# Kernel tuning notes

Hardware: AMD Instinct MI355X
Metric: run time of the kernel (lower is better)

Reference implementation:

```python
import jax, jax.numpy as jnp
import numpy as np

N_HEADS = 16
HIDDEN = 1024
HEAD_DIM = 64
BSZ = 4
SEQ = 1024
SCALE = HEAD_DIM ** -0.5


def setup_inputs() -> dict:
    key = jax.random.key(0)
    k_x, k_q, k_k, k_v, k_o = jax.random.split(key, 5)
    s = HIDDEN ** -0.5
    return {
        "x": jax.random.normal(k_x, (BSZ, SEQ, HIDDEN), dtype=jnp.float32),
        # torch nn.Linear weights: shape (out_features, in_features)
        "wq": jax.random.normal(k_q, (N_HEADS * HEAD_DIM, HIDDEN), dtype=jnp.float32) * s,
        "wk": jax.random.normal(k_k, (N_HEADS * HEAD_DIM, HIDDEN), dtype=jnp.float32) * s,
        "wv": jax.random.normal(k_v, (N_HEADS * HEAD_DIM, HIDDEN), dtype=jnp.float32) * s,
        "wo": jax.random.normal(k_o, (HIDDEN, N_HEADS * HEAD_DIM), dtype=jnp.float32) * s,
    }


def reference(x, wq, wk, wv, wo):
    bsz, seqlen, _ = x.shape
    xq = jnp.einsum("bsh,oh->bso", x, wq)  # (b, s, n_heads*head_dim)
    xk = jnp.einsum("bsh,oh->bso", x, wk)
    xv = jnp.einsum("bsh,oh->bso", x, wv)
    # Faithful to the original: raw view to (b, n_heads, s, head_dim), NO transpose
    xq = xq.reshape(bsz, N_HEADS, seqlen, HEAD_DIM)
    xk = xk.reshape(bsz, N_HEADS, seqlen, HEAD_DIM)
    xv = xv.reshape(bsz, N_HEADS, seqlen, HEAD_DIM)
    scores = jnp.einsum("bhid,bhjd->bhij", xq, xk) * SCALE
    scores = jax.nn.softmax(scores, axis=-1)
    out = jnp.einsum("bhij,bhjd->bhid", scores, xv)
    out = out.reshape(bsz, seqlen, N_HEADS * HEAD_DIM)  # raw view, faithful
    return jnp.einsum("bso,ho->bsh", out, wo)
```

## Files before the change

kernel.cpp:

```cpp
#include <hip/hip_runtime.h>
#include <hip/hip_bf16.h>

typedef __hip_bfloat16 bf16;
typedef __attribute__((ext_vector_type(8))) short short8;
typedef __attribute__((ext_vector_type(4))) short short4v;
typedef __attribute__((ext_vector_type(4))) float f32x4;


__device__ __forceinline__ short f2b(float x) {
    bf16 h = __float2bfloat16(x);
    return *reinterpret_cast<short*>(&h);
}
__device__ __forceinline__ f32x4 zero4() {
    f32x4 z; z[0] = 0.f; z[1] = 0.f; z[2] = 0.f; z[3] = 0.f; return z;
}
__device__ __forceinline__ void gl_lds16(const void* g, void* l) {
    __builtin_amdgcn_global_load_lds(
        (const __attribute__((address_space(1))) void*)g,
        (__attribute__((address_space(3))) void*)l, 16, 0, 0);
}

__global__ __launch_bounds__(256) void convert_in(const float* __restrict__ w0,
                                                  const float* __restrict__ w1,
                                                  const float* __restrict__ w2,
                                                  const float* __restrict__ w3,
                                                  const float* __restrict__ x,
                                                  bf16* __restrict__ Wb,
                                                  bf16* __restrict__ Xb) {
    const int y = blockIdx.y;
    const float* s;
    bf16* d;
    if (y < 4) {
        s = (y == 0) ? w0 : (y == 1) ? w1 : (y == 2) ? w2 : w3;
        d = Wb + (size_t)y * 1048576;
    } else {
        s = x + (size_t)(y - 4) * 1048576;
        d = Xb + (size_t)(y - 4) * 1048576;
    }
    const int i = (blockIdx.x * 256 + threadIdx.x) * 4;
    const float4 v = *(const float4*)(s + i);
    short4v o;
    o[0] = f2b(v.x); o[1] = f2b(v.y); o[2] = f2b(v.z); o[3] = f2b(v.w);
    *(short4v*)(d + i) = o;
}

__global__ __launch_bounds__(256) void gemm_qkv(const bf16* __restrict__ Xb,
                                                const bf16* __restrict__ Wb,
                                                bf16* __restrict__ QK,
                                                bf16* __restrict__ VT) {
    __shared__ __align__(16) bf16 As[128 * 32];
    __shared__ __align__(16) bf16 Bs[128 * 32];

    const int tid  = threadIdx.x;
    const int wave = tid >> 6;
    const int lane = tid & 63;
    const int z    = blockIdx.z;
    const int bm   = blockIdx.x * 128, bn = blockIdx.y * 128;
    const bf16* Bsrc = Wb + (size_t)z * 1048576;

    const int f0 = wave * 2048 + lane * 16, f1 = f0 + 1024;
    const char* gA0 = (const char*)(Xb + (size_t)(bm + (f0 >> 6)) * 1024) + (f0 & 63);
    const char* gA1 = (const char*)(Xb + (size_t)(bm + (f1 >> 6)) * 1024) + (f1 & 63);
    const char* gB0 = (const char*)(Bsrc + (size_t)(bn + (f0 >> 6)) * 1024) + (f0 & 63);
    const char* gB1 = (const char*)(Bsrc + (size_t)(bn + (f1 >> 6)) * 1024) + (f1 & 63);
    char* lA0 = (char*)As + wave * 2048;      char* lA1 = lA0 + 1024;
    char* lB0 = (char*)Bs + wave * 2048;      char* lB1 = lB0 + 1024;

    f32x4 acc[4][4];
#pragma unroll
    for (int i = 0; i < 4; i++)
#pragma unroll
        for (int j = 0; j < 4; j++) acc[i][j] = zero4();

    const int mrow = ((wave >> 1) * 64) + (lane & 15);
    const int nrow = ((wave & 1) * 64) + (lane & 15);
    const int kcol = (lane >> 4) * 8;

    for (int k0 = 0; k0 < 1024; k0 += 32) {
        __syncthreads();
        gl_lds16(gA0 + (size_t)k0 * 2, lA0);
        gl_lds16(gA1 + (size_t)k0 * 2, lA1);
        gl_lds16(gB0 + (size_t)k0 * 2, lB0);
        gl_lds16(gB1 + (size_t)k0 * 2, lB1);
        __syncthreads();
        short8 af[4], bfr[4];
#pragma unroll
        for (int i = 0; i < 4; i++)
            af[i] = *(const short8*)&As[(mrow + i * 16) * 32 + kcol];
#pragma unroll
        for (int j = 0; j < 4; j++)
            bfr[j] = *(const short8*)&Bs[(nrow + j * 16) * 32 + kcol];
#pragma unroll
        for (int i = 0; i < 4; i++)
#pragma unroll
            for (int j = 0; j < 4; j++)
                acc[i][j] = __builtin_amdgcn_mfma_f32_16x16x32_bf16(
                    af[i], bfr[j], acc[i][j], 0, 0, 0);
    }

    const int erow = bm + (wave >> 1) * 64 + (lane >> 4) * 4;
    const int ecol = bn + (wave & 1) * 64 + (lane & 15);
    if (z < 2) {
        bf16* C = QK + (size_t)z * 4194304;
#pragma unroll
        for (int i = 0; i < 4; i++)
#pragma unroll
            for (int j = 0; j < 4; j++)
#pragma unroll
                for (int r = 0; r < 4; r++)
                    C[(size_t)(erow + i * 16 + r) * 1024 + (ecol + j * 16)] =
                        __float2bfloat16(acc[i][j][r]);
    } else {
#pragma unroll
        for (int i = 0; i < 4; i++)
#pragma unroll
            for (int j = 0; j < 4; j++) {
                const int o  = ecol + j * 16;
                const int d  = o & 63;
                const int oh = o >> 6;
#pragma unroll
                for (int r = 0; r < 4; r++) {
                    const int rr = erow + i * 16 + r;
                    VT[(size_t)(rr >> 6) * 65536 + d * 1024 +
                       ((rr & 63) * 16 + oh)] = __float2bfloat16(acc[i][j][r]);
                }
            }
    }
}

__global__ __launch_bounds__(256) void gemm_out(const bf16* __restrict__ A,
                                                const bf16* __restrict__ B,
                                                float* __restrict__ C) {
    __shared__ __align__(16) bf16 As[128 * 32];
    __shared__ __align__(16) bf16 Bs[64 * 32];

    const int tid  = threadIdx.x;
    const int wave = tid >> 6;
    const int lane = tid & 63;
    const int bm   = blockIdx.x * 128, bn = blockIdx.y * 64;

    const int f0 = wave * 2048 + lane * 16, f1 = f0 + 1024;
    const int fB = tid * 16;
    const char* gA0 = (const char*)(A + (size_t)(bm + (f0 >> 6)) * 1024) + (f0 & 63);
    const char* gA1 = (const char*)(A + (size_t)(bm + (f1 >> 6)) * 1024) + (f1 & 63);
    const char* gB0 = (const char*)(B + (size_t)(bn + (fB >> 6)) * 1024) + (fB & 63);
    char* lA0 = (char*)As + f0;
    char* lA1 = (char*)As + f1;
    char* lB0 = (char*)Bs + fB;

    f32x4 acc[4][2];
#pragma unroll
    for (int i = 0; i < 4; i++)
#pragma unroll
        for (int j = 0; j < 2; j++) acc[i][j] = zero4();

    const int mrow = ((wave >> 1) * 64) + (lane & 15);
    const int nrow = ((wave & 1) * 32) + (lane & 15);
    const int kcol = (lane >> 4) * 8;

    for (int k0 = 0; k0 < 1024; k0 += 32) {
        __syncthreads();
        gl_lds16(gA0 + (size_t)k0 * 2, lA0);
        gl_lds16(gA1 + (size_t)k0 * 2, lA1);
        gl_lds16(gB0 + (size_t)k0 * 2, lB0);
        __syncthreads();
        short8 af[4], bfr[2];
#pragma unroll
        for (int i = 0; i < 4; i++)
            af[i] = *(const short8*)&As[(mrow + i * 16) * 32 + kcol];
#pragma unroll
        for (int j = 0; j < 2; j++)
            bfr[j] = *(const short8*)&Bs[(nrow + j * 16) * 32 + kcol];
#pragma unroll
        for (int i = 0; i < 4; i++)
#pragma unroll
            for (int j = 0; j < 2; j++)
                acc[i][j] = __builtin_amdgcn_mfma_f32_16x16x32_bf16(
                    af[i], bfr[j], acc[i][j], 0, 0, 0);
    }

    const int erow = bm + (wave >> 1) * 64 + (lane >> 4) * 4;
    const int ecol = bn + (wave & 1) * 32 + (lane & 15);
#pragma unroll
    for (int i = 0; i < 4; i++)
#pragma unroll
        for (int j = 0; j < 2; j++)
#pragma unroll
            for (int r = 0; r < 4; r++)
                C[(size_t)(erow + i * 16 + r) * 1024 + (ecol + j * 16)] =
                    acc[i][j][r];
}

#define PSTR 72
__global__ __launch_bounds__(256) void attn(bf16* __restrict__ QO,
                                            const bf16* __restrict__ K,
                                            const bf16* __restrict__ VT) {
    __shared__ __align__(16) bf16 Ks[64 * 64];
    __shared__ __align__(16) bf16 Vs[64 * 64];
    __shared__ __align__(16) bf16 Ps[128 * PSTR];

    const int tid  = threadIdx.x;
    const int wave = tid >> 6;
    const int lane = tid & 63;
    const int lg   = lane >> 4;
    const int li   = lane & 15;

    const int head = blockIdx.x >> 3;
    const int qt   = blockIdx.x & 7;
    bf16* Qh = QO + (size_t)head * 65536 + qt * 8192;
    const char* Khb  = (const char*)(K + (size_t)head * 65536);
    const char* VThb = (const char*)(VT + (size_t)head * 65536);

    short8 qf[2][2];
#pragma unroll
    for (int i = 0; i < 2; i++)
#pragma unroll
        for (int ks = 0; ks < 2; ks++)
            qf[i][ks] = *(const short8*)&Qh[(wave * 32 + i * 16 + li) * 64 +
                                            ks * 32 + lg * 8];

    f32x4 o_acc[2][4];
    float lp[2][4];
#pragma unroll
    for (int i = 0; i < 2; i++) {
#pragma unroll
        for (int j = 0; j < 4; j++) o_acc[i][j] = zero4();
#pragma unroll
        for (int r = 0; r < 4; r++) lp[i][r] = 0.f;
    }

    const int fs0 = wave * 2048 + lane * 16, fs1 = fs0 + 1024;
    char* lK0 = (char*)Ks + fs0;   char* lK1 = (char*)Ks + fs1;
    char* lV0 = (char*)Vs + fs0;   char* lV1 = (char*)Vs + fs1;
    const char* gV0 = VThb + (size_t)(fs0 >> 7) * 2048 + (fs0 & 127);
    const char* gV1 = VThb + (size_t)(fs1 >> 7) * 2048 + (fs1 & 127);

    for (int jt = 0; jt < 16; jt++) {
        __syncthreads();
        gl_lds16(Khb + (size_t)jt * 8192 + fs0, lK0);
        gl_lds16(Khb + (size_t)jt * 8192 + fs1, lK1);
        gl_lds16(gV0 + jt * 128, lV0);
        gl_lds16(gV1 + jt * 128, lV1);
        __syncthreads();

        f32x4 s_acc[2][4];
#pragma unroll
        for (int i = 0; i < 2; i++)
#pragma unroll
            for (int j = 0; j < 4; j++) s_acc[i][j] = zero4();
#pragma unroll
        for (int j = 0; j < 4; j++)
#pragma unroll
            for (int ks = 0; ks < 2; ks++) {
                short8 kf = *(const short8*)&Ks[(j * 16 + li) * 64 + ks * 32 + lg * 8];
#pragma unroll
                for (int i = 0; i < 2; i++)
                    s_acc[i][j] = __builtin_amdgcn_mfma_f32_16x16x32_bf16(
                        qf[i][ks], kf, s_acc[i][j], 0, 0, 0);
            }

#pragma unroll
        for (int i = 0; i < 2; i++)
#pragma unroll
            for (int r = 0; r < 4; r++) {
                const int prow = wave * 32 + i * 16 + lg * 4 + r;
                float ps = 0.f;
#pragma unroll
                for (int j = 0; j < 4; j++) {
                    const float p = __expf(s_acc[i][j][r] * 0.125f);
                    ps += p;
                    Ps[prow * PSTR + j * 16 + li] = __float2bfloat16(p);
                }
                lp[i][r] += ps;
            }

#pragma unroll
        for (int ks = 0; ks < 2; ks++) {
            short8 pa[2];
#pragma unroll
            for (int i = 0; i < 2; i++)
                pa[i] = *(const short8*)&Ps[(wave * 32 + i * 16 + li) * PSTR +
                                            ks * 32 + lg * 8];
#pragma unroll
            for (int jd = 0; jd < 4; jd++) {
                short8 vf = *(const short8*)&Vs[(jd * 16 + li) * 64 + ks * 32 + lg * 8];
#pragma unroll
                for (int i = 0; i < 2; i++)
                    o_acc[i][jd] = __builtin_amdgcn_mfma_f32_16x16x32_bf16(
                        pa[i], vf, o_acc[i][jd], 0, 0, 0);
            }
        }
    }

#pragma unroll
    for (int i = 0; i < 2; i++)
#pragma unroll
        for (int r = 0; r < 4; r++) {
            float l = lp[i][r];
#pragma unroll
            for (int off = 1; off < 16; off <<= 1) l += __shfl_xor(l, off, 16);
            const float inv = 1.f / l;
#pragma unroll
            for (int jd = 0; jd < 4; jd++)
                Qh[(wave * 32 + i * 16 + lg * 4 + r) * 64 + jd * 16 + li] =
                    __float2bfloat16(o_acc[i][jd][r] * inv);
        }
}

extern "C" void kernel_launch(void* const* d_in, const int* in_sizes, int n_in,
                              void* d_out, int out_size, void* d_ws, size_t ws_size,
                              hipStream_t stream) {
    const float* x  = (const float*)d_in[0];
    const float* wq = (const float*)d_in[1];
    const float* wk = (const float*)d_in[2];
    const float* wv = (const float*)d_in[3];
    const float* wo = (const float*)d_in[4];

    bf16* ws = (bf16*)d_ws;
    bf16* Wb = ws;
    bf16* QK = ws + 4194304;
    bf16* VT = ws + 12582912;
    bf16* Xb = (bf16*)d_out;

    convert_in<<<dim3(1024, 8), 256, 0, stream>>>(wq, wk, wv, wo, x, Wb, Xb);
    gemm_qkv<<<dim3(32, 8, 3), 256, 0, stream>>>(Xb, Wb, QK, VT);
    attn<<<512, 256, 0, stream>>>(QK, QK + 4194304, VT);
    gemm_out<<<dim3(32, 16), 256, 0, stream>>>(QK, Wb + 3145728, (float*)d_out);
}
```

Baseline: 188.7 us.

## Rewrite QKV GEMM as 256x256 8-wave kernel with double-buffered swizzled LDS

Replaces the 128x128 QKV projection GEMM with a 256x256-tile, 512-thread kernel that double-buffers 64-wide K slices in 128KB of LDS. It uses an XOR swizzle to avoid bank conflicts and splits each K step into four phases that interleave global-to-LDS prefetch with MFMA work, using manual barriers, waitcnts and setprio. The goal is to overlap memory latency with compute and raise data reuse per block compared with the fully synchronous single-buffer loop. The trade-off is a much smaller grid (192 blocks), heavy register and LDS use that may limit occupancy, and fragile hand-written synchronisation.

```diff
diff --git a/kernel.cpp b/kernel.cpp
--- a/kernel.cpp
+++ b/kernel.cpp
@@ -44,87 +44,128 @@
     *(short4v*)(d + i) = o;
 }
 
-__global__ __launch_bounds__(256) void gemm_qkv(const bf16* __restrict__ Xb,
-                                                const bf16* __restrict__ Wb,
-                                                bf16* __restrict__ QK,
-                                                bf16* __restrict__ VT) {
-    __shared__ __align__(16) bf16 As[128 * 32];
-    __shared__ __align__(16) bf16 Bs[128 * 32];
+#define PH(MQ, NQ, READA, SG, SLOFF, VM) do {                                  \
+    if (READA) {                                                               \
+      _Pragma("unroll") for (int i = 0; i < 4; ++i)                            \
+      _Pragma("unroll") for (int ks = 0; ks < 2; ++ks)                         \
+        af[i][ks] = *(const short8*)(ldsb + d + (MQ)*16384 +                   \
+            (((wr*64 + i*16 + li)*64 + ((ks*32 + lg*8) ^ swz)) << 1));         \
+    }                                                                          \
+    _Pragma("unroll") for (int j = 0; j < 2; ++j)                              \
+    _Pragma("unroll") for (int ks = 0; ks < 2; ++ks)                           \
+      bfr[j][ks] = *(const short8*)(ldsb + d + 32768 + (NQ)*16384 +            \
+          (((wc*32 + j*16 + li)*64 + ((ks*32 + lg*8) ^ swz)) << 1));           \
+    gl_lds16(SG + (size_t)ktn * 64, ldsw + dn + (SLOFF));                      \
+    gl_lds16(SG + (size_t)ktn * 64 + 65536, ldsw + dn + (SLOFF) + 8192);       \
+    asm volatile("" ::: "memory");                                             \
+    __builtin_amdgcn_s_barrier();                                              \
+    asm volatile("s_waitcnt lgkmcnt(0)" ::: "memory");                         \
+    __builtin_amdgcn_sched_barrier(0);                                         \
+    __builtin_amdgcn_s_setprio(1);                                             \
+    _Pragma("unroll") for (int i = 0; i < 4; ++i)                              \
+    _Pragma("unroll") for (int j = 0; j < 2; ++j)                              \
+    _Pragma("unroll") for (int ks = 0; ks < 2; ++ks)                           \
+      acc[(MQ)*4 + i][(NQ)*2 + j] = __builtin_amdgcn_mfma_f32_16x16x32_bf16(   \
+          af[i][ks], bfr[j][ks], acc[(MQ)*4 + i][(NQ)*2 + j], 0, 0, 0);        \
+    __builtin_amdgcn_s_setprio(0);                                             \
+    if (VM) asm volatile("s_waitcnt vmcnt(4)" ::: "memory");                   \
+    __builtin_amdgcn_s_barrier();                                              \
+  } while (0)
+
+__global__ __launch_bounds__(512, 2) void gemm_qkv8(const bf16* __restrict__ Xb,
+                                                    const bf16* __restrict__ Wb,
+                                                    bf16* __restrict__ QK,
+                                                    bf16* __restrict__ VT) {
+    __shared__ __align__(16) bf16 lds[65536];
 
     const int tid  = threadIdx.x;
-    const int wave = tid >> 6;
+    const int w    = tid >> 6;
     const int lane = tid & 63;
+    const int wr   = w >> 2;
+    const int wc   = w & 3;
+    const int li   = lane & 15;
+    const int lg   = lane >> 4;
+    const int swz  = (li & 7) << 3;
     const int z    = blockIdx.z;
-    const int bm   = blockIdx.x * 128, bn = blockIdx.y * 128;
+    const int bm   = blockIdx.x * 256, bn = blockIdx.y * 256;
     const bf16* Bsrc = Wb + (size_t)z * 1048576;
 
-    const int f0 = wave * 2048 + lane * 16, f1 = f0 + 1024;
-    const char* gA0 = (const char*)(Xb + (size_t)(bm + (f0 >> 6)) * 1024) + (f0 & 63);
-    const char* gA1 = (const char*)(Xb + (size_t)(bm + (f1 >> 6)) * 1024) + (f1 & 63);
-    const char* gB0 = (const char*)(Bsrc + (size_t)(bn + (f0 >> 6)) * 1024) + (f0 & 63);
-    const char* gB1 = (const char*)(Bsrc + (size_t)(bn + (f1 >> 6)) * 1024) + (f1 & 63);
-    char* lA0 = (char*)As + wave * 2048;      char* lA1 = lA0 + 1024;
-    char* lB0 = (char*)Bs + wave * 2048;      char* lB1 = lB0 + 1024;
-
-    f32x4 acc[4][4];
-#pragma unroll
-    for (int i = 0; i < 4; i++)
-#pragma unroll
-        for (int j = 0; j < 4; j++) acc[i][j] = zero4();
-
-    const int mrow = ((wave >> 1) * 64) + (lane & 15);
-    const int nrow = ((wave & 1) * 64) + (lane & 15);
-    const int kcol = (lane >> 4) * 8;
-
-    for (int k0 = 0; k0 < 1024; k0 += 32) {
-        __syncthreads();
-        gl_lds16(gA0 + (size_t)k0 * 2, lA0);
-        gl_lds16(gA1 + (size_t)k0 * 2, lA1);
-        gl_lds16(gB0 + (size_t)k0 * 2, lB0);
-        gl_lds16(gB1 + (size_t)k0 * 2, lB1);
-        __syncthreads();
-        short8 af[4], bfr[4];
-#pragma unroll
-        for (int i = 0; i < 4; i++)
-            af[i] = *(const short8*)&As[(mrow + i * 16) * 32 + kcol];
-#pragma unroll
-        for (int j = 0; j < 4; j++)
-            bfr[j] = *(const short8*)&Bs[(nrow + j * 16) * 32 + kcol];
-#pragma unroll
-        for (int i = 0; i < 4; i++)
-#pragma unroll
-            for (int j = 0; j < 4; j++)
-                acc[i][j] = __builtin_amdgcn_mfma_f32_16x16x32_bf16(
-                    af[i], bfr[j], acc[i][j], 0, 0, 0);
-    }
-
-    const int erow = bm + (wave >> 1) * 64 + (lane >> 4) * 4;
-    const int ecol = bn + (wave & 1) * 64 + (lane & 15);
+    const int srow = w * 8 + (lane >> 3);
+    const int scol = ((lane & 7) ^ (lane >> 3)) * 8;
+    const bf16* gA0 = Xb   + (size_t)(bm + srow) * 1024 + scol;
+    const bf16* gB0 = Bsrc + (size_t)(bn + srow) * 1024 + scol;
+    const bf16* gA1 = gA0 + 131072;
+    const bf16* gB1 = gB0 + 131072;
+    const char* ldsb = (const char*)lds;
+    char* ldsw = (char*)lds + w * 1024;
+
+    f32x4 acc[8][4];
+#pragma unroll
+    for (int i = 0; i < 8; ++i)
+#pragma unroll
+        for (int j = 0; j < 4; ++j) acc[i][j] = zero4();
+
+    short8 af[4][2], bfr[2][2];
+
+    {
+        gl_lds16(gA0, ldsw + 0);      gl_lds16(gA0 + 65536, ldsw + 8192);
+        gl_lds16(gB0, ldsw + 32768);  gl_lds16(gB0 + 65536, ldsw + 40960);
+        gl_lds16(gB1, ldsw + 49152);  gl_lds16(gB1 + 65536, ldsw + 57344);
+        gl_lds16(gA1, ldsw + 16384);  gl_lds16(gA1 + 65536, ldsw + 24576);
+        asm volatile("s_waitcnt vmcnt(4)" ::: "memory");
+        __builtin_amdgcn_s_barrier();
+    }
+
+    for (int kt = 0; kt < 16; ++kt) {
+        const int d   = (kt & 1) << 16;
+        const int dn  = ((kt + 1) & 1) << 16;
+        const int ktn = (kt < 15) ? kt + 1 : 0;
+        PH(0, 0, 1, gA0, 0,     1);
+        PH(0, 1, 0, gB0, 32768, 1);
+        PH(1, 0, 1, gB1, 49152, 0);
+        PH(1, 1, 0, gA1, 16384, 1);
+    }
+
+    asm volatile("s_waitcnt vmcnt(0)" ::: "memory");
+
     if (z < 2) {
         bf16* C = QK + (size_t)z * 4194304;
 #pragma unroll
-        for (int i = 0; i < 4; i++)
-#pragma unroll
-            for (int j = 0; j < 4; j++)
-#pragma unroll
-                for (int r = 0; r < 4; r++)
-                    C[(size_t)(erow + i * 16 + r) * 1024 + (ecol + j * 16)] =
-                        __float2bfloat16(acc[i][j][r]);
+        for (int mq = 0; mq < 2; ++mq)
+#pragma unroll
+        for (int i = 0; i < 4; ++i)
+#pragma unroll
+        for (int nq = 0; nq < 2; ++nq)
+#pragma unroll
+        for (int j = 0; j < 2; ++j) {
+            const int gr0 = bm + mq * 128 + wr * 64 + i * 16 + lg * 4;
+            const int gc  = bn + nq * 128 + wc * 32 + j * 16 + li;
+#pragma unroll
+            for (int r = 0; r < 4; ++r)
+                C[(size_t)(gr0 + r) * 1024 + gc] =
+                    __float2bfloat16(acc[mq * 4 + i][nq * 2 + j][r]);
+        }
     } else {
 #pragma unroll
-        for (int i = 0; i < 4; i++)
-#pragma unroll
-            for (int j = 0; j < 4; j++) {
-                const int o  = ecol + j * 16;
-                const int d  = o & 63;
-                const int oh = o >> 6;
-#pragma unroll
-                for (int r = 0; r < 4; r++) {
-                    const int rr = erow + i * 16 + r;
-                    VT[(size_t)(rr >> 6) * 65536 + d * 1024 +
-                       ((rr & 63) * 16 + oh)] = __float2bfloat16(acc[i][j][r]);
-                }
+        for (int mq = 0; mq < 2; ++mq)
+#pragma unroll
+        for (int i = 0; i < 4; ++i)
+#pragma unroll
+        for (int nq = 0; nq < 2; ++nq)
+#pragma unroll
+        for (int j = 0; j < 2; ++j) {
+            const int gr0 = bm + mq * 128 + wr * 64 + i * 16 + lg * 4;
+            const int o   = bn + nq * 128 + wc * 32 + j * 16 + li;
+            const int dd  = o & 63;
+            const int oh  = o >> 6;
+#pragma unroll
+            for (int r = 0; r < 4; ++r) {
+                const int rr = gr0 + r;
+                VT[(size_t)(rr >> 6) * 65536 + dd * 1024 +
+                   ((rr & 63) * 16 + oh)] =
+                    __float2bfloat16(acc[mq * 4 + i][nq * 2 + j][r]);
             }
+        }
     }
 }
 
@@ -323,7 +364,7 @@
     bf16* Xb = (bf16*)d_out;
 
     convert_in<<<dim3(1024, 8), 256, 0, stream>>>(wq, wk, wv, wo, x, Wb, Xb);
-    gemm_qkv<<<dim3(32, 8, 3), 256, 0, stream>>>(Xb, Wb, QK, VT);
+    gemm_qkv8<<<dim3(16, 4, 3), 512, 0, stream>>>(Xb, Wb, QK, VT);
     attn<<<512, 256, 0, stream>>>(QK, QK + 4194304, VT);
     gemm_out<<<dim3(32, 16), 256, 0, stream>>>(QK, Wb + 3145728, (float*)d_out);
 }
```

After: 204.7 us. 1.08x slower.

## Triple-buffer LDS tiles in QKV and output GEMMs with async prefetch

Applied to the files above, without the earlier changes.

Both GEMM kernels now keep three LDS stages and issue global-to-LDS loads two k-tiles ahead. A partial vmcnt wait plus a single barrier per iteration replaces the two __syncthreads, so loads can overlap the MFMA work. The cost is triple the LDS footprint per block, which may lower occupancy. The loads wrap around to k-tile 0/1 at the end, doing redundant work that is only drained afterwards.

```diff
diff --git a/kernel.cpp b/kernel.cpp
--- a/kernel.cpp
+++ b/kernel.cpp
@@ -48,8 +48,8 @@
                                                 const bf16* __restrict__ Wb,
                                                 bf16* __restrict__ QK,
                                                 bf16* __restrict__ VT) {
-    __shared__ __align__(16) bf16 As[128 * 32];
-    __shared__ __align__(16) bf16 Bs[128 * 32];
+    __shared__ __align__(16) bf16 As[3][128 * 32];
+    __shared__ __align__(16) bf16 Bs[3][128 * 32];
 
     const int tid  = threadIdx.x;
     const int wave = tid >> 6;
@@ -63,8 +63,15 @@
     const char* gA1 = (const char*)(Xb + (size_t)(bm + (f1 >> 6)) * 1024) + (f1 & 63);
     const char* gB0 = (const char*)(Bsrc + (size_t)(bn + (f0 >> 6)) * 1024) + (f0 & 63);
     const char* gB1 = (const char*)(Bsrc + (size_t)(bn + (f1 >> 6)) * 1024) + (f1 & 63);
-    char* lA0 = (char*)As + wave * 2048;      char* lA1 = lA0 + 1024;
-    char* lB0 = (char*)Bs + wave * 2048;      char* lB1 = lB0 + 1024;
+    char* Ab = (char*)As;
+    char* Bb = (char*)Bs;
+
+#define QKV_STAGE(BUF, KB) do {                                   \
+        gl_lds16(gA0 + (KB), Ab + (BUF) + f0);                    \
+        gl_lds16(gA1 + (KB), Ab + (BUF) + f1);                    \
+        gl_lds16(gB0 + (KB), Bb + (BUF) + f0);                    \
+        gl_lds16(gB1 + (KB), Bb + (BUF) + f1);                    \
+    } while (0)
 
     f32x4 acc[4][4];
 #pragma unroll
@@ -76,27 +83,35 @@
     const int nrow = ((wave & 1) * 64) + (lane & 15);
     const int kcol = (lane >> 4) * 8;
 
-    for (int k0 = 0; k0 < 1024; k0 += 32) {
-        __syncthreads();
-        gl_lds16(gA0 + (size_t)k0 * 2, lA0);
-        gl_lds16(gA1 + (size_t)k0 * 2, lA1);
-        gl_lds16(gB0 + (size_t)k0 * 2, lB0);
-        gl_lds16(gB1 + (size_t)k0 * 2, lB1);
-        __syncthreads();
+    QKV_STAGE(0, 0);
+    QKV_STAGE(8192, 64);
+
+    int bR = 0, bS = 16384;
+    for (int kt = 0; kt < 32; ++kt) {
+        asm volatile("s_waitcnt vmcnt(4)" ::: "memory");
+        __builtin_amdgcn_s_barrier();
+        const int kb = ((kt + 2) & 31) * 64;
+        QKV_STAGE(bS, kb);
         short8 af[4], bfr[4];
 #pragma unroll
         for (int i = 0; i < 4; i++)
-            af[i] = *(const short8*)&As[(mrow + i * 16) * 32 + kcol];
+            af[i] = *(const short8*)(Ab + bR +
+                        (((mrow + i * 16) * 32 + kcol) << 1));
 #pragma unroll
         for (int j = 0; j < 4; j++)
-            bfr[j] = *(const short8*)&Bs[(nrow + j * 16) * 32 + kcol];
+            bfr[j] = *(const short8*)(Bb + bR +
+                        (((nrow + j * 16) * 32 + kcol) << 1));
 #pragma unroll
         for (int i = 0; i < 4; i++)
 #pragma unroll
             for (int j = 0; j < 4; j++)
                 acc[i][j] = __builtin_amdgcn_mfma_f32_16x16x32_bf16(
                     af[i], bfr[j], acc[i][j], 0, 0, 0);
-    }
+        bR = (bR == 16384) ? 0 : bR + 8192;
+        bS = (bS == 16384) ? 0 : bS + 8192;
+    }
+    asm volatile("s_waitcnt vmcnt(0)" ::: "memory");
+#undef QKV_STAGE
 
     const int erow = bm + (wave >> 1) * 64 + (lane >> 4) * 4;
     const int ecol = bn + (wave & 1) * 64 + (lane & 15);
@@ -131,8 +146,8 @@
 __global__ __launch_bounds__(256) void gemm_out(const bf16* __restrict__ A,
                                                 const bf16* __restrict__ B,
                                                 float* __restrict__ C) {
-    __shared__ __align__(16) bf16 As[128 * 32];
-    __shared__ __align__(16) bf16 Bs[64 * 32];
+    __shared__ __align__(16) bf16 As[3][128 * 32];
+    __shared__ __align__(16) bf16 Bs[3][64 * 32];
 
     const int tid  = threadIdx.x;
     const int wave = tid >> 6;
@@ -144,9 +159,14 @@
     const char* gA0 = (const char*)(A + (size_t)(bm + (f0 >> 6)) * 1024) + (f0 & 63);
     const char* gA1 = (const char*)(A + (size_t)(bm + (f1 >> 6)) * 1024) + (f1 & 63);
     const char* gB0 = (const char*)(B + (size_t)(bn + (fB >> 6)) * 1024) + (fB & 63);
-    char* lA0 = (char*)As + f0;
-    char* lA1 = (char*)As + f1;
-    char* lB0 = (char*)Bs + fB;
+    char* Ab = (char*)As;
+    char* Bb = (char*)Bs;
+
+#define OUT_STAGE(BA, BB, KB) do {                                \
+        gl_lds16(gA0 + (KB), Ab + (BA) + f0);                     \
+        gl_lds16(gA1 + (KB), Ab + (BA) + f1);                     \
+        gl_lds16(gB0 + (KB), Bb + (BB) + fB);                     \
+    } while (0)
 
     f32x4 acc[4][2];
 #pragma unroll
@@ -158,26 +178,38 @@
     const int nrow = ((wave & 1) * 32) + (lane & 15);
     const int kcol = (lane >> 4) * 8;
 
-    for (int k0 = 0; k0 < 1024; k0 += 32) {
-        __syncthreads();
-        gl_lds16(gA0 + (size_t)k0 * 2, lA0);
-        gl_lds16(gA1 + (size_t)k0 * 2, lA1);
-        gl_lds16(gB0 + (size_t)k0 * 2, lB0);
-        __syncthreads();
+    OUT_STAGE(0, 0, 0);
+    OUT_STAGE(8192, 4096, 64);
+
+    int aR = 0, aS = 16384;
+    int bBR = 0, bBS = 8192;
+    for (int kt = 0; kt < 32; ++kt) {
+        asm volatile("s_waitcnt vmcnt(3)" ::: "memory");
+        __builtin_amdgcn_s_barrier();
+        const int kb = ((kt + 2) & 31) * 64;
+        OUT_STAGE(aS, bBS, kb);
         short8 af[4], bfr[2];
 #pragma unroll
         for (int i = 0; i < 4; i++)
-            af[i] = *(const short8*)&As[(mrow + i * 16) * 32 + kcol];
+            af[i] = *(const short8*)(Ab + aR +
+                        (((mrow + i * 16) * 32 + kcol) << 1));
 #pragma unroll
         for (int j = 0; j < 2; j++)
-            bfr[j] = *(const short8*)&Bs[(nrow + j * 16) * 32 + kcol];
+            bfr[j] = *(const short8*)(Bb + bBR +
+                        (((nrow + j * 16) * 32 + kcol) << 1));
 #pragma unroll
         for (int i = 0; i < 4; i++)
 #pragma unroll
             for (int j = 0; j < 2; j++)
                 acc[i][j] = __builtin_amdgcn_mfma_f32_16x16x32_bf16(
                     af[i], bfr[j], acc[i][j], 0, 0, 0);
-    }
+        aR  = (aR == 16384) ? 0 : aR + 8192;
+        aS  = (aS == 16384) ? 0 : aS + 8192;
+        bBR = (bBR == 8192) ? 0 : bBR + 4096;
+        bBS = (bBS == 8192) ? 0 : bBS + 4096;
+    }
+    asm volatile("s_waitcnt vmcnt(0)" ::: "memory");
+#undef OUT_STAGE
 
     const int erow = bm + (wave >> 1) * 64 + (lane >> 4) * 4;
     const int ecol = bn + (wave & 1) * 32 + (lane & 15);
```

After: 192.1 us. No clear change (+1.8%).

## Double-buffer K/V tiles in attention and remap block-to-head order

Applied to the files above, without the earlier changes.

The attention kernel now keeps two LDS buffers for K and V and issues the async global-to-LDS loads for the next key tile before computing on the current one. It uses a partial vmcnt wait so that the next tile's fetch overlaps with the MFMA and softmax work. Block indices are also permuted so that consecutive blocks fall on different heads, spreading concurrent blocks across heads, which may change L2 locality. The extra LDS raises per-block shared memory use, which could lower occupancy, and the last iteration issues a redundant load of tile 15.

```diff
diff --git a/kernel.cpp b/kernel.cpp
--- a/kernel.cpp
+++ b/kernel.cpp
@@ -195,8 +195,8 @@
 __global__ __launch_bounds__(256) void attn(bf16* __restrict__ QO,
                                             const bf16* __restrict__ K,
                                             const bf16* __restrict__ VT) {
-    __shared__ __align__(16) bf16 Ks[64 * 64];
-    __shared__ __align__(16) bf16 Vs[64 * 64];
+    __shared__ __align__(16) bf16 Ks[2][64 * 64];
+    __shared__ __align__(16) bf16 Vs[2][64 * 64];
     __shared__ __align__(16) bf16 Ps[128 * PSTR];
 
     const int tid  = threadIdx.x;
@@ -205,8 +205,9 @@
     const int lg   = lane >> 4;
     const int li   = lane & 15;
 
-    const int head = blockIdx.x >> 3;
-    const int qt   = blockIdx.x & 7;
+    const int bid  = blockIdx.x;
+    const int head = ((bid & 7) << 3) | ((bid >> 3) & 7);
+    const int qt   = bid >> 6;
     bf16* Qh = QO + (size_t)head * 65536 + qt * 8192;
     const char* Khb  = (const char*)(K + (size_t)head * 65536);
     const char* VThb = (const char*)(VT + (size_t)head * 65536);
@@ -230,18 +231,32 @@
     }
 
     const int fs0 = wave * 2048 + lane * 16, fs1 = fs0 + 1024;
-    char* lK0 = (char*)Ks + fs0;   char* lK1 = (char*)Ks + fs1;
-    char* lV0 = (char*)Vs + fs0;   char* lV1 = (char*)Vs + fs1;
+    char* KsB = (char*)Ks;
+    char* VsB = (char*)Vs;
     const char* gV0 = VThb + (size_t)(fs0 >> 7) * 2048 + (fs0 & 127);
     const char* gV1 = VThb + (size_t)(fs1 >> 7) * 2048 + (fs1 & 127);
 
+    gl_lds16(Khb + fs0, KsB + fs0);
+    gl_lds16(Khb + fs1, KsB + fs1);
+    gl_lds16(gV0, VsB + fs0);
+    gl_lds16(gV1, VsB + fs1);
+
     for (int jt = 0; jt < 16; jt++) {
-        __syncthreads();
-        gl_lds16(Khb + (size_t)jt * 8192 + fs0, lK0);
-        gl_lds16(Khb + (size_t)jt * 8192 + fs1, lK1);
-        gl_lds16(gV0 + jt * 128, lV0);
-        gl_lds16(gV1 + jt * 128, lV1);
-        __syncthreads();
+        const int p  = (jt & 1) * 8192;
+        const int pn = 8192 - p;
+        const int jn = (jt < 15) ? jt + 1 : 15;
+        asm volatile("" ::: "memory");
+        __builtin_amdgcn_s_barrier();
+        gl_lds16(Khb + (size_t)jn * 8192 + fs0, KsB + pn + fs0);
+        gl_lds16(Khb + (size_t)jn * 8192 + fs1, KsB + pn + fs1);
+        gl_lds16(gV0 + jn * 128, VsB + pn + fs0);
+        gl_lds16(gV1 + jn * 128, VsB + pn + fs1);
+        asm volatile("s_waitcnt vmcnt(4)" ::: "memory");
+        __builtin_amdgcn_s_barrier();
+        asm volatile("" ::: "memory");
+
+        const bf16* Kc = (const bf16*)(KsB + p);
+        const bf16* Vc = (const bf16*)(VsB + p);
 
         f32x4 s_acc[2][4];
 #pragma unroll
@@ -252,7 +267,7 @@
         for (int j = 0; j < 4; j++)
 #pragma unroll
             for (int ks = 0; ks < 2; ks++) {
-                short8 kf = *(const short8*)&Ks[(j * 16 + li) * 64 + ks * 32 + lg * 8];
+                short8 kf = *(const short8*)&Kc[(j * 16 + li) * 64 + ks * 32 + lg * 8];
 #pragma unroll
                 for (int i = 0; i < 2; i++)
                     s_acc[i][j] = __builtin_amdgcn_mfma_f32_16x16x32_bf16(
@@ -267,9 +282,9 @@
                 float ps = 0.f;
 #pragma unroll
                 for (int j = 0; j < 4; j++) {
-                    const float p = __expf(s_acc[i][j][r] * 0.125f);
-                    ps += p;
-                    Ps[prow * PSTR + j * 16 + li] = __float2bfloat16(p);
+                    const float pv = __expf(s_acc[i][j][r] * 0.125f);
+                    ps += pv;
+                    Ps[prow * PSTR + j * 16 + li] = __float2bfloat16(pv);
                 }
                 lp[i][r] += ps;
             }
@@ -283,7 +298,7 @@
                                             ks * 32 + lg * 8];
 #pragma unroll
             for (int jd = 0; jd < 4; jd++) {
-                short8 vf = *(const short8*)&Vs[(jd * 16 + li) * 64 + ks * 32 + lg * 8];
+                short8 vf = *(const short8*)&Vc[(jd * 16 + li) * 64 + ks * 32 + lg * 8];
 #pragma unroll
                 for (int i = 0; i < 2; i++)
                     o_acc[i][jd] = __builtin_amdgcn_mfma_f32_16x16x32_bf16(
@@ -291,6 +306,7 @@
             }
         }
     }
+    asm volatile("s_waitcnt vmcnt(0)" ::: "memory");
 
 #pragma unroll
     for (int i = 0; i < 2; i++)
```

After: 184.1 us. -2.4%, faster.
